# Kernel tuning notes

Hardware: AMD Instinct MI355X
Metric: run time of the kernel (lower is better)

The kernel has to match this reference:

```python
import jax, jax.numpy as jnp
import numpy as np

D_IN, D, K, N_CLASSES = 384, 512, 6, 2
SCALE = D ** (-0.5)

def _linear_params(key, fan_in, fan_out):
    kw, kb = jax.random.split(key)
    w = jax.random.normal(kw, (fan_in, fan_out), jnp.float32) * 0.02
    b = jax.random.normal(kb, (fan_out,), jnp.float32) * 0.01
    return w, b

def setup_inputs() -> dict:
    key = jax.random.key(0)
    ks = jax.random.split(key, 10)
    x = jax.random.normal(ks[0], (16384, D_IN), jnp.float32)
    fc1_w, fc1_b = _linear_params(ks[1], D_IN, D)
    wh_w, wh_b = _linear_params(ks[2], D, D)
    wt_w, wt_b = _linear_params(ks[3], D, D)
    lin1_w, lin1_b = _linear_params(ks[4], D, D)
    lin2_w, lin2_b = _linear_params(ks[5], D, D)
    att1_w, att1_b = _linear_params(ks[6], D, D // 2)
    att2_w, att2_b = _linear_params(ks[7], D // 2, 1)
    ln_g = jnp.ones((D,), jnp.float32)
    ln_b = jnp.zeros((D,), jnp.float32)
    fc_w, fc_b = _linear_params(ks[8], D, N_CLASSES)
    return dict(x=x, fc1_w=fc1_w, fc1_b=fc1_b, wh_w=wh_w, wh_b=wh_b,
                wt_w=wt_w, wt_b=wt_b, lin1_w=lin1_w, lin1_b=lin1_b,
                lin2_w=lin2_w, lin2_b=lin2_b, att1_w=att1_w, att1_b=att1_b,
                att2_w=att2_w, att2_b=att2_b, ln_g=ln_g, ln_b=ln_b,
                fc_w=fc_w, fc_b=fc_b)

def _forward(x, fc1_w, fc1_b, wh_w, wh_b, wt_w, wt_b, lin1_w, lin1_b,
             lin2_w, lin2_b, att1_w, att1_b, att2_w, att2_b, ln_g, ln_b,
             fc_w, fc_b):
    lrelu = jax.nn.leaky_relu  # slope 0.01, matches nn.LeakyReLU default
    h = lrelu(x @ fc1_w + fc1_b)                    # [N, D]
    h = (h + h.mean(axis=0, keepdims=True)) * 0.5
    e_h = h @ wh_w + wh_b                           # [N, D]
    e_t = h @ wt_w + wt_b                           # [N, D]
    attn_logit = (e_h * SCALE) @ e_t.T              # [N, N]
    topk_w, topk_i = jax.lax.top_k(attn_logit, K)   # [N, K]
    Nb = e_t[topk_i]                                # gather neighbors [N, K, D]
    p = jax.nn.softmax(topk_w, axis=-1)             # [N, K]
    eh_r = p[..., None] * Nb + (1.0 - p)[..., None] * e_h[:, None, :]
    gate = jnp.tanh(e_h[:, None, :] + eh_r)         # [N, K, D]
    # faithful to torch.einsum('ijkl,ijkm->ijk', Nb, gate): product of sums
    ka_w = Nb.sum(axis=-1) * gate.sum(axis=-1)      # [N, K]
    ka_p = jax.nn.softmax(ka_w, axis=-1)
    e_Nh = jnp.einsum('nk,nkd->nd', ka_p, Nb)       # [N, D]
    sum_emb = lrelu((e_h + e_Nh) @ lin1_w + lin1_b)
    bi_emb = lrelu((e_h * e_Nh) @ lin2_w + lin2_b)
    emb = sum_emb + bi_emb                          # [N, D] (dropout=eval, identity)
    # GlobalAttention readout
    a = lrelu(emb @ att1_w + att1_b) @ att2_w + att2_b  # [N, 1]
    g = jax.nn.softmax(a, axis=0)
    pooled = (g * emb).sum(axis=0, keepdims=True)   # [1, D]
    mu = pooled.mean(axis=-1, keepdims=True)
    var = pooled.var(axis=-1, keepdims=True)
    normed = (pooled - mu) * jax.lax.rsqrt(var + 1e-5) * ln_g + ln_b
    logits = normed @ fc_w + fc_b                   # [1, n_classes]
    return logits

def reference(x, fc1_w, fc1_b, wh_w, wh_b, wt_w, wt_b, lin1_w, lin1_b,
              lin2_w, lin2_b, att1_w, att1_b, att2_w, att2_b, ln_g, ln_b,
              fc_w, fc_b):
    logits = _forward(x, fc1_w, fc1_b, wh_w, wh_b, wt_w, wt_b, lin1_w, lin1_b,
                      lin2_w, lin2_b, att1_w, att1_b, att2_w, att2_b,
                      ln_g, ln_b, fc_w, fc_b)
    y_prob = jax.nn.softmax(logits, axis=-1)
    return logits, y_prob
```

## Files before the change

### kernel.cpp

```cpp
#include <hip/hip_runtime.h>
#include <math.h>

#define NROWS 16384
#define DIN   384
#define DIM   512
#define KSEL  6
#define NSPLIT 4
#define COLS_PER_SPLIT (NROWS / NSPLIT)
#define ATT_SCALE 0.044194173824159216f

typedef unsigned short u16;
typedef __attribute__((ext_vector_type(8))) short bf16x8;
typedef __attribute__((ext_vector_type(16))) float f32x16;

static __device__ __forceinline__ float lrelu_f(float v) {
  return v > 0.f ? v : 0.01f * v;
}

static __device__ __forceinline__ u16 f2bf(float f) {
  unsigned u = __float_as_uint(f);
  unsigned r = (u + 0x7FFFu + ((u >> 16) & 1u)) >> 16;
  return (u16)r;
}

static __device__ __forceinline__ float bf2f(u16 v) {
  return __uint_as_float(((unsigned)v) << 16);
}

static __device__ __forceinline__ void sbar() {
  asm volatile("" ::: "memory");
  __builtin_amdgcn_s_barrier();
  asm volatile("" ::: "memory");
}

static __device__ __forceinline__ void wconv_body(const float* W, u16* Wt,
                                                  int K, int N, int t) {
  if (t >= K * N) return;
  int k = t / N, n = t - k * N;
  Wt[(size_t)n * K + k] = f2bf(W[t]);
}

__global__ __launch_bounds__(256)
void prep(const float* __restrict__ X, u16* __restrict__ Xb,
          const float* __restrict__ fc1_w, u16* __restrict__ fc1t,
          const float* __restrict__ wh_w, u16* __restrict__ wht,
          const float* __restrict__ wt_w, u16* __restrict__ wtt,
          const float* __restrict__ lin1_w, u16* __restrict__ lin1t,
          const float* __restrict__ lin2_w, u16* __restrict__ lin2t,
          const float* __restrict__ att1_w, u16* __restrict__ att1t) {
  const int b = blockIdx.x, tid = threadIdx.x;
  if (b < 3072) {
    int i = b * 256 + tid;
    const float4* p = (const float4*)X + (size_t)i * 2;
    float4 a = p[0], c = p[1];
    uint4 o;
    o.x = f2bf(a.x) | ((unsigned)f2bf(a.y) << 16);
    o.y = f2bf(a.z) | ((unsigned)f2bf(a.w) << 16);
    o.z = f2bf(c.x) | ((unsigned)f2bf(c.y) << 16);
    o.w = f2bf(c.z) | ((unsigned)f2bf(c.w) << 16);
    ((uint4*)Xb)[i] = o;
  } else if (b < 3840) {
    wconv_body(fc1_w, fc1t, 384, 512, (b - 3072) * 256 + tid);
  } else if (b < 4864) {
    wconv_body(wh_w, wht, 512, 512, (b - 3840) * 256 + tid);
  } else if (b < 5888) {
    wconv_body(wt_w, wtt, 512, 512, (b - 4864) * 256 + tid);
  } else if (b < 6912) {
    wconv_body(lin1_w, lin1t, 512, 512, (b - 5888) * 256 + tid);
  } else if (b < 7936) {
    wconv_body(lin2_w, lin2t, 512, 512, (b - 6912) * 256 + tid);
  } else {
    wconv_body(att1_w, att1t, 512, 256, (b - 7936) * 256 + tid);
  }
}

__global__ __launch_bounds__(256)
void colsum_partial(const float* __restrict__ H, float* __restrict__ part) {
  int col = blockIdx.x * 64 + (threadIdx.x & 63);
  int sub = threadIdx.x >> 6;
  int rEnd = blockIdx.y * 512 + 512;
  float s = 0.f;
  for (int r = blockIdx.y * 512 + sub; r < rEnd; r += 4)
    s += H[(size_t)r * DIM + col];
  __shared__ float sh[4][64];
  sh[sub][threadIdx.x & 63] = s;
  __syncthreads();
  if (threadIdx.x < 64) {
    float tot = sh[0][threadIdx.x] + sh[1][threadIdx.x] +
                sh[2][threadIdx.x] + sh[3][threadIdx.x];
    part[(size_t)blockIdx.y * DIM + col] = tot;
  }
}

__global__ void finalize_mean(const float* __restrict__ part,
                              float* __restrict__ mean) {
  int c = threadIdx.x;
  float s = 0.f;
  for (int j = 0; j < 32; j++) s += part[j * DIM + c];
  mean[c] = s * (1.0f / NROWS);
}

__global__ __launch_bounds__(256)
void h_fix_bf(const float* __restrict__ H0, const float* __restrict__ mean,
              u16* __restrict__ Hb) {
  int idx = blockIdx.x * 256 + threadIdx.x;
  int c = (idx * 8) & (DIM - 1);
  const float4* p = (const float4*)H0 + (size_t)idx * 2;
  float4 a = p[0], b = p[1];
  float4 m0 = *(const float4*)(mean + c);
  float4 m1 = *(const float4*)(mean + c + 4);
  a.x = (a.x + m0.x) * 0.5f; a.y = (a.y + m0.y) * 0.5f;
  a.z = (a.z + m0.z) * 0.5f; a.w = (a.w + m0.w) * 0.5f;
  b.x = (b.x + m1.x) * 0.5f; b.y = (b.y + m1.y) * 0.5f;
  b.z = (b.z + m1.z) * 0.5f; b.w = (b.w + m1.w) * 0.5f;
  uint4 o;
  o.x = f2bf(a.x) | ((unsigned)f2bf(a.y) << 16);
  o.y = f2bf(a.z) | ((unsigned)f2bf(a.w) << 16);
  o.z = f2bf(b.x) | ((unsigned)f2bf(b.y) << 16);
  o.w = f2bf(b.z) | ((unsigned)f2bf(b.w) << 16);
  ((uint4*)Hb)[idx] = o;
}

template<int ACT, int STOREBF, int STOREF32>
__global__ __launch_bounds__(256, 2)
void gemm_bf16(const u16* __restrict__ A, const u16* __restrict__ Wt,
               const float* __restrict__ bias, float* __restrict__ C,
               u16* __restrict__ Cb, float bscale, int K, int N) {
  __shared__ char lds[65536];
  const int tid = threadIdx.x;
  const int w = tid >> 6, l = tid & 63;
  const int l31 = l & 31, lh = l >> 5, lh16 = lh << 4;
  const int qg = w & 1, ng = w >> 1;
  const int swz = (l31 & 7) << 4;
  const int rowBase = blockIdx.y * 128;
  const int colBase = blockIdx.x * 128;
  const int nsteps = K >> 6;

  f32x16 z;
  #pragma unroll
  for (int i = 0; i < 16; i++) z[i] = 0.f;
  f32x16 acc00 = z, acc01 = z, acc10 = z, acc11 = z;

#define GSTAGE(buf_, kc_) do { \
    const int r_ = tid >> 3, j_ = tid & 7; \
    const int js_ = ((j_ ^ (r_ & 7)) << 3); \
    const u16* as_ = A + (size_t)rowBase * K + (kc_); \
    const u16* ws_ = Wt + (size_t)colBase * K + (kc_); \
    char* ab_ = lds + (buf_) * 16384; \
    char* wb_ = lds + 32768 + (buf_) * 16384; \
    _Pragma("unroll") \
    for (int p_ = 0; p_ < 4; ++p_) { \
      __builtin_amdgcn_global_load_lds( \
        (const __attribute__((address_space(1))) void*)(as_ + (size_t)(r_ + 32 * p_) * K + js_), \
        (__attribute__((address_space(3))) void*)(ab_ + w * 1024 + p_ * 4096), 16, 0, 0); \
      __builtin_amdgcn_global_load_lds( \
        (const __attribute__((address_space(1))) void*)(ws_ + (size_t)(r_ + 32 * p_) * K + js_), \
        (__attribute__((address_space(3))) void*)(wb_ + w * 1024 + p_ * 4096), 16, 0, 0); \
    } \
  } while (0)

  GSTAGE(0, 0);
  asm volatile("s_waitcnt vmcnt(0)" ::: "memory");
  sbar();
  #pragma unroll 1
  for (int s = 0; s < nsteps; ++s) {
    const int cur = s & 1;
    if (s + 1 < nsteps) GSTAGE(cur ^ 1, (s + 1) * 64);
    __builtin_amdgcn_sched_barrier(0);
    const char* ab = lds + cur * 16384;
    const char* wb = lds + 32768 + cur * 16384;
    __builtin_amdgcn_s_setprio(1);
    #pragma unroll
    for (int s4 = 0; s4 < 4; ++s4) {
      const int off = (s4 * 32 + lh16) ^ swz;
      bf16x8 am0 = *(const bf16x8*)(ab + (qg * 64 + l31) * 128 + off);
      bf16x8 am1 = *(const bf16x8*)(ab + (qg * 64 + 32 + l31) * 128 + off);
      bf16x8 wn0 = *(const bf16x8*)(wb + (ng * 64 + l31) * 128 + off);
      bf16x8 wn1 = *(const bf16x8*)(wb + (ng * 64 + 32 + l31) * 128 + off);
      acc00 = __builtin_amdgcn_mfma_f32_32x32x16_bf16(wn0, am0, acc00, 0, 0, 0);
      acc01 = __builtin_amdgcn_mfma_f32_32x32x16_bf16(wn1, am0, acc01, 0, 0, 0);
      acc10 = __builtin_amdgcn_mfma_f32_32x32x16_bf16(wn0, am1, acc10, 0, 0, 0);
      acc11 = __builtin_amdgcn_mfma_f32_32x32x16_bf16(wn1, am1, acc11, 0, 0, 0);
    }
    __builtin_amdgcn_s_setprio(0);
    asm volatile("s_waitcnt vmcnt(0)" ::: "memory");
    sbar();
  }
#undef GSTAGE

  float* Ls = (float*)lds;
  {
    const int m0 = qg * 64 + l31;
    const int k0 = (m0 & 7) << 2;
    #pragma unroll
    for (int r = 0; r < 16; ++r) {
      const int nd = ng * 64 + (r & 3) + 8 * (r >> 2) + 4 * lh;
      Ls[m0 * 128 + (nd ^ k0)] = acc00[r];
      Ls[m0 * 128 + ((nd + 32) ^ k0)] = acc01[r];
      Ls[(m0 + 32) * 128 + (nd ^ k0)] = acc10[r];
      Ls[(m0 + 32) * 128 + ((nd + 32) ^ k0)] = acc11[r];
    }
  }
  sbar();
  #pragma unroll
  for (int p = 0; p < 16; ++p) {
    int idx = tid + 256 * p;
    int m = idx >> 5, c4 = (idx & 31) << 2;
    float4 v = *(const float4*)&Ls[m * 128 + (c4 ^ ((m & 7) << 2))];
    int col = colBase + c4;
    float4 bv = *(const float4*)&bias[col];
    v.x += bv.x; v.y += bv.y; v.z += bv.z; v.w += bv.w;
    if (ACT) {
      v.x = lrelu_f(v.x); v.y = lrelu_f(v.y);
      v.z = lrelu_f(v.z); v.w = lrelu_f(v.w);
    }
    size_t o = (size_t)(rowBase + m) * N + col;
    if (STOREF32) *(float4*)&C[o] = v;
    if (STOREBF) {
      ushort4 q;
      q.x = f2bf(v.x * bscale); q.y = f2bf(v.y * bscale);
      q.z = f2bf(v.z * bscale); q.w = f2bf(v.w * bscale);
      *(ushort4*)&Cb[o] = q;
    }
  }
}

__global__ __launch_bounds__(256, 2)
void gemm_dualA(const u16* __restrict__ A, const u16* __restrict__ W1t,
                const u16* __restrict__ W2t,
                const float* __restrict__ b1, const float* __restrict__ b2,
                u16* __restrict__ C1b, u16* __restrict__ C2b) {
  __shared__ char lds[65536];
  const int tid = threadIdx.x;
  const int w = tid >> 6, l = tid & 63;
  const int l31 = l & 31, lh = l >> 5, lh16 = lh << 4;
  const int qg = w & 1, ng = w >> 1;
  const int swz = (l31 & 7) << 4;
  const int rowBase = blockIdx.y * 128;
  const int colBase = blockIdx.x * 128;

  f32x16 z;
  #pragma unroll
  for (int i = 0; i < 16; i++) z[i] = 0.f;
  f32x16 p00 = z, p01 = z, p10 = z, p11 = z;
  f32x16 q00 = z, q01 = z, q10 = z, q11 = z;

  #pragma unroll 1
  for (int s = 0; s < 8; ++s) {
    {
      const int r_ = tid >> 3, j_ = tid & 7;
      const int js_ = ((j_ ^ (r_ & 7)) << 3);
      const u16* as_ = A + (size_t)rowBase * DIM + s * 64;
      const u16* w1_ = W1t + (size_t)colBase * DIM + s * 64;
      const u16* w2_ = W2t + (size_t)colBase * DIM + s * 64;
      #pragma unroll
      for (int p_ = 0; p_ < 4; ++p_) {
        __builtin_amdgcn_global_load_lds(
          (const __attribute__((address_space(1))) void*)(as_ + (size_t)(r_ + 32 * p_) * DIM + js_),
          (__attribute__((address_space(3))) void*)(lds + w * 1024 + p_ * 4096), 16, 0, 0);
        __builtin_amdgcn_global_load_lds(
          (const __attribute__((address_space(1))) void*)(w1_ + (size_t)(r_ + 32 * p_) * DIM + js_),
          (__attribute__((address_space(3))) void*)(lds + 16384 + w * 1024 + p_ * 4096), 16, 0, 0);
        __builtin_amdgcn_global_load_lds(
          (const __attribute__((address_space(1))) void*)(w2_ + (size_t)(r_ + 32 * p_) * DIM + js_),
          (__attribute__((address_space(3))) void*)(lds + 32768 + w * 1024 + p_ * 4096), 16, 0, 0);
      }
    }
    asm volatile("s_waitcnt vmcnt(0)" ::: "memory");
    sbar();
    const char* ab = lds;
    const char* w1b = lds + 16384;
    const char* w2b = lds + 32768;
    __builtin_amdgcn_s_setprio(1);
    #pragma unroll
    for (int s4 = 0; s4 < 4; ++s4) {
      const int off = (s4 * 32 + lh16) ^ swz;
      bf16x8 am0 = *(const bf16x8*)(ab + (qg * 64 + l31) * 128 + off);
      bf16x8 am1 = *(const bf16x8*)(ab + (qg * 64 + 32 + l31) * 128 + off);
      bf16x8 x0 = *(const bf16x8*)(w1b + (ng * 64 + l31) * 128 + off);
      bf16x8 x1 = *(const bf16x8*)(w1b + (ng * 64 + 32 + l31) * 128 + off);
      bf16x8 y0 = *(const bf16x8*)(w2b + (ng * 64 + l31) * 128 + off);
      bf16x8 y1 = *(const bf16x8*)(w2b + (ng * 64 + 32 + l31) * 128 + off);
      p00 = __builtin_amdgcn_mfma_f32_32x32x16_bf16(x0, am0, p00, 0, 0, 0);
      p01 = __builtin_amdgcn_mfma_f32_32x32x16_bf16(x1, am0, p01, 0, 0, 0);
      p10 = __builtin_amdgcn_mfma_f32_32x32x16_bf16(x0, am1, p10, 0, 0, 0);
      p11 = __builtin_amdgcn_mfma_f32_32x32x16_bf16(x1, am1, p11, 0, 0, 0);
      q00 = __builtin_amdgcn_mfma_f32_32x32x16_bf16(y0, am0, q00, 0, 0, 0);
      q01 = __builtin_amdgcn_mfma_f32_32x32x16_bf16(y1, am0, q01, 0, 0, 0);
      q10 = __builtin_amdgcn_mfma_f32_32x32x16_bf16(y0, am1, q10, 0, 0, 0);
      q11 = __builtin_amdgcn_mfma_f32_32x32x16_bf16(y1, am1, q11, 0, 0, 0);
    }
    __builtin_amdgcn_s_setprio(0);
    sbar();
  }

  float* Ls = (float*)lds;
  const int m0 = qg * 64 + l31;
  const int k0 = (m0 & 7) << 2;
  #pragma unroll
  for (int r = 0; r < 16; ++r) {
    const int nd = ng * 64 + (r & 3) + 8 * (r >> 2) + 4 * lh;
    Ls[m0 * 128 + (nd ^ k0)] = p00[r];
    Ls[m0 * 128 + ((nd + 32) ^ k0)] = p01[r];
    Ls[(m0 + 32) * 128 + (nd ^ k0)] = p10[r];
    Ls[(m0 + 32) * 128 + ((nd + 32) ^ k0)] = p11[r];
  }
  sbar();
  #pragma unroll
  for (int p = 0; p < 16; ++p) {
    int idx = tid + 256 * p;
    int m = idx >> 5, c4 = (idx & 31) << 2;
    float4 v = *(const float4*)&Ls[m * 128 + (c4 ^ ((m & 7) << 2))];
    int col = colBase + c4;
    float4 bv = *(const float4*)&b1[col];
    v.x += bv.x; v.y += bv.y; v.z += bv.z; v.w += bv.w;
    size_t o = (size_t)(rowBase + m) * DIM + col;
    ushort4 qo;
    qo.x = f2bf(v.x); qo.y = f2bf(v.y); qo.z = f2bf(v.z); qo.w = f2bf(v.w);
    *(ushort4*)&C1b[o] = qo;
  }
  sbar();
  #pragma unroll
  for (int r = 0; r < 16; ++r) {
    const int nd = ng * 64 + (r & 3) + 8 * (r >> 2) + 4 * lh;
    Ls[m0 * 128 + (nd ^ k0)] = q00[r];
    Ls[m0 * 128 + ((nd + 32) ^ k0)] = q01[r];
    Ls[(m0 + 32) * 128 + (nd ^ k0)] = q10[r];
    Ls[(m0 + 32) * 128 + ((nd + 32) ^ k0)] = q11[r];
  }
  sbar();
  #pragma unroll
  for (int p = 0; p < 16; ++p) {
    int idx = tid + 256 * p;
    int m = idx >> 5, c4 = (idx & 31) << 2;
    float4 v = *(const float4*)&Ls[m * 128 + (c4 ^ ((m & 7) << 2))];
    int col = colBase + c4;
    float4 bv = *(const float4*)&b2[col];
    v.x += bv.x; v.y += bv.y; v.z += bv.z; v.w += bv.w;
    size_t o = (size_t)(rowBase + m) * DIM + col;
    ushort4 qo;
    qo.x = f2bf(v.x); qo.y = f2bf(v.y); qo.z = f2bf(v.z); qo.w = f2bf(v.w);
    *(ushort4*)&C2b[o] = qo;
  }
}

__global__ __launch_bounds__(256, 2)
void gemm_dualsum(const u16* __restrict__ A1, const u16* __restrict__ A2,
                  const u16* __restrict__ W1t, const u16* __restrict__ W2t,
                  const float* __restrict__ b1, const float* __restrict__ b2,
                  u16* __restrict__ Cb) {
  __shared__ char lds[65536];
  const int tid = threadIdx.x;
  const int w = tid >> 6, l = tid & 63;
  const int l31 = l & 31, lh = l >> 5, lh16 = lh << 4;
  const int qg = w & 1, ng = w >> 1;
  const int swz = (l31 & 7) << 4;
  const int rowBase = blockIdx.y * 128;
  const int colBase = blockIdx.x * 128;

  f32x16 z;
  #pragma unroll
  for (int i = 0; i < 16; i++) z[i] = 0.f;
  f32x16 p00 = z, p01 = z, p10 = z, p11 = z;
  f32x16 q00 = z, q01 = z, q10 = z, q11 = z;

  #pragma unroll 1
  for (int s = 0; s < 8; ++s) {
    {
      const int r_ = tid >> 3, j_ = tid & 7;
      const int js_ = ((j_ ^ (r_ & 7)) << 3);
      const u16* a1_ = A1 + (size_t)rowBase * DIM + s * 64;
      const u16* a2_ = A2 + (size_t)rowBase * DIM + s * 64;
      const u16* w1_ = W1t + (size_t)colBase * DIM + s * 64;
      const u16* w2_ = W2t + (size_t)colBase * DIM + s * 64;
      #pragma unroll
      for (int p_ = 0; p_ < 4; ++p_) {
        __builtin_amdgcn_global_load_lds(
          (const __attribute__((address_space(1))) void*)(a1_ + (size_t)(r_ + 32 * p_) * DIM + js_),
          (__attribute__((address_space(3))) void*)(lds + w * 1024 + p_ * 4096), 16, 0, 0);
        __builtin_amdgcn_global_load_lds(
          (const __attribute__((address_space(1))) void*)(a2_ + (size_t)(r_ + 32 * p_) * DIM + js_),
          (__attribute__((address_space(3))) void*)(lds + 16384 + w * 1024 + p_ * 4096), 16, 0, 0);
        __builtin_amdgcn_global_load_lds(
          (const __attribute__((address_space(1))) void*)(w1_ + (size_t)(r_ + 32 * p_) * DIM + js_),
          (__attribute__((address_space(3))) void*)(lds + 32768 + w * 1024 + p_ * 4096), 16, 0, 0);
        __builtin_amdgcn_global_load_lds(
          (const __attribute__((address_space(1))) void*)(w2_ + (size_t)(r_ + 32 * p_) * DIM + js_),
          (__attribute__((address_space(3))) void*)(lds + 49152 + w * 1024 + p_ * 4096), 16, 0, 0);
      }
    }
    asm volatile("s_waitcnt vmcnt(0)" ::: "memory");
    sbar();
    const char* a1b = lds;
    const char* a2b = lds + 16384;
    const char* w1b = lds + 32768;
    const char* w2b = lds + 49152;
    __builtin_amdgcn_s_setprio(1);
    #pragma unroll
    for (int s4 = 0; s4 < 4; ++s4) {
      const int off = (s4 * 32 + lh16) ^ swz;
      bf16x8 am0 = *(const bf16x8*)(a1b + (qg * 64 + l31) * 128 + off);
      bf16x8 am1 = *(const bf16x8*)(a1b + (qg * 64 + 32 + l31) * 128 + off);
      bf16x8 bm0 = *(const bf16x8*)(a2b + (qg * 64 + l31) * 128 + off);
      bf16x8 bm1 = *(const bf16x8*)(a2b + (qg * 64 + 32 + l31) * 128 + off);
      bf16x8 x0 = *(const bf16x8*)(w1b + (ng * 64 + l31) * 128 + off);
      bf16x8 x1 = *(const bf16x8*)(w1b + (ng * 64 + 32 + l31) * 128 + off);
      bf16x8 y0 = *(const bf16x8*)(w2b + (ng * 64 + l31) * 128 + off);
      bf16x8 y1 = *(const bf16x8*)(w2b + (ng * 64 + 32 + l31) * 128 + off);
      p00 = __builtin_amdgcn_mfma_f32_32x32x16_bf16(x0, am0, p00, 0, 0, 0);
      p01 = __builtin_amdgcn_mfma_f32_32x32x16_bf16(x1, am0, p01, 0, 0, 0);
      p10 = __builtin_amdgcn_mfma_f32_32x32x16_bf16(x0, am1, p10, 0, 0, 0);
      p11 = __builtin_amdgcn_mfma_f32_32x32x16_bf16(x1, am1, p11, 0, 0, 0);
      q00 = __builtin_amdgcn_mfma_f32_32x32x16_bf16(y0, bm0, q00, 0, 0, 0);
      q01 = __builtin_amdgcn_mfma_f32_32x32x16_bf16(y1, bm0, q01, 0, 0, 0);
      q10 = __builtin_amdgcn_mfma_f32_32x32x16_bf16(y0, bm1, q10, 0, 0, 0);
      q11 = __builtin_amdgcn_mfma_f32_32x32x16_bf16(y1, bm1, q11, 0, 0, 0);
    }
    __builtin_amdgcn_s_setprio(0);
    sbar();
  }

  float* Ls = (float*)lds;
  const int m0 = qg * 64 + l31;
  const int k0 = (m0 & 7) << 2;
  #pragma unroll
  for (int r = 0; r < 16; ++r) {
    const int nd = ng * 64 + (r & 3) + 8 * (r >> 2) + 4 * lh;
    const int c0 = colBase + nd, c1 = colBase + nd + 32;
    Ls[m0 * 128 + (nd ^ k0)] =
        lrelu_f(p00[r] + b1[c0]) + lrelu_f(q00[r] + b2[c0]);
    Ls[m0 * 128 + ((nd + 32) ^ k0)] =
        lrelu_f(p01[r] + b1[c1]) + lrelu_f(q01[r] + b2[c1]);
    Ls[(m0 + 32) * 128 + (nd ^ k0)] =
        lrelu_f(p10[r] + b1[c0]) + lrelu_f(q10[r] + b2[c0]);
    Ls[(m0 + 32) * 128 + ((nd + 32) ^ k0)] =
        lrelu_f(p11[r] + b1[c1]) + lrelu_f(q11[r] + b2[c1]);
  }
  sbar();
  #pragma unroll
  for (int p = 0; p < 16; ++p) {
    int idx = tid + 256 * p;
    int m = idx >> 5, c4 = (idx & 31) << 2;
    float4 v = *(const float4*)&Ls[m * 128 + (c4 ^ ((m & 7) << 2))];
    int col = colBase + c4;
    size_t o = (size_t)(rowBase + m) * DIM + col;
    ushort4 qo;
    qo.x = f2bf(v.x); qo.y = f2bf(v.y); qo.z = f2bf(v.z); qo.w = f2bf(v.w);
    *(ushort4*)&Cb[o] = qo;
  }
}

#define T6(tv, tix, vv, cc) do { float v_ = (vv); \
  if (v_ > tv[5]) { tv[5] = v_; tix[5] = (cc); \
    if (tv[5] > tv[4]) { float t=tv[4];tv[4]=tv[5];tv[5]=t; int q=tix[4];tix[4]=tix[5];tix[5]=q; } \
    if (tv[4] > tv[3]) { float t=tv[3];tv[3]=tv[4];tv[4]=t; int q=tix[3];tix[3]=tix[4];tix[4]=q; } \
    if (tv[3] > tv[2]) { float t=tv[2];tv[2]=tv[3];tv[3]=t; int q=tix[2];tix[2]=tix[3];tix[3]=q; } \
    if (tv[2] > tv[1]) { float t=tv[1];tv[1]=tv[2];tv[2]=t; int q=tix[1];tix[1]=tix[2];tix[2]=q; } \
    if (tv[1] > tv[0]) { float t=tv[0];tv[0]=tv[1];tv[1]=t; int q=tix[0];tix[0]=tix[1];tix[1]=q; } \
  } } while (0)

__global__ __launch_bounds__(256, 2)
void attn_topk_mfma(const u16* __restrict__ EHb, const u16* __restrict__ ETb,
                    float* __restrict__ TWp, int* __restrict__ TIp) {
  __shared__ char lds[49152];
  const int tid = threadIdx.x;
  const int w = tid >> 6, l = tid & 63;
  const int l31 = l & 31, lh = l >> 5;

  const int bid = blockIdx.x;
  const int xcd = bid & 7;
  const int split = xcd & 3;
  const int rowBase = ((xcd >> 2) * 64 + (bid >> 3)) * 128;
  const int qrow = rowBase + w * 32 + l31;

  bf16x8 areg[32];
  {
    const u16* ap = EHb + (size_t)qrow * DIM + lh * 8;
    #pragma unroll
    for (int ks = 0; ks < 32; ++ks)
      areg[ks] = *(const bf16x8*)(ap + ks * 16);
  }

  f32x16 z;
  #pragma unroll
  for (int i = 0; i < 16; i++) z[i] = 0.f;
  f32x16 acc0 = z, acc1 = z;

  float tv[KSEL]; int tix[KSEL];
  #pragma unroll
  for (int k = 0; k < KSEL; k++) { tv[k] = -INFINITY; tix[k] = 0x7fffffff; }

#define STAGE(bufi_, ph_) do { \
    const int ct_ = (ph_) >> 2, kc_ = (ph_) & 3; \
    char* db_ = lds + (bufi_) * 16384; \
    const u16* bs_ = ETb + (size_t)(split * COLS_PER_SPLIT + ct_ * 64) * DIM + kc_ * 128; \
    _Pragma("unroll") \
    for (int p_ = 0; p_ < 4; ++p_) { \
      const int c_ = (w * 4 + p_) * 64 + l; \
      const int rn_ = c_ >> 4; \
      const int js_ = ((c_ & 15) ^ (rn_ & 15)) << 3; \
      __builtin_amdgcn_global_load_lds( \
        (const __attribute__((address_space(1))) void*)(bs_ + (size_t)rn_ * DIM + js_), \
        (__attribute__((address_space(3))) void*)(db_ + (w * 4 + p_) * 1024), 16, 0, 0); \
    } \
  } while (0)

  int bufr = 0;
  STAGE(0, 0);
  STAGE(1, 1);
  asm volatile("s_waitcnt vmcnt(4)" ::: "memory");

  #pragma unroll 1
  for (int ct = 0; ct < 64; ++ct) {
    #pragma unroll
    for (int kc = 0; kc < 4; ++kc) {
      sbar();
      const char* db = lds + bufr * 16384;
      __builtin_amdgcn_s_setprio(1);
      #pragma unroll
      for (int s = 0; s < 8; ++s) {
        const int j0 = ((s * 2 + lh) ^ (l31 & 15)) * 16;
        bf16x8 bn0 = *(const bf16x8*)(db + l31 * 256 + j0);
        const int r1 = 32 + l31;
        const int j1 = ((s * 2 + lh) ^ (r1 & 15)) * 16;
        bf16x8 bn1 = *(const bf16x8*)(db + r1 * 256 + j1);
        acc0 = __builtin_amdgcn_mfma_f32_32x32x16_bf16(bn0, areg[kc * 8 + s], acc0, 0, 0, 0);
        acc1 = __builtin_amdgcn_mfma_f32_32x32x16_bf16(bn1, areg[kc * 8 + s], acc1, 0, 0, 0);
      }
      __builtin_amdgcn_s_setprio(0);
      if (kc == 3) {
        const int cb = split * COLS_PER_SPLIT + ct * 64 + 4 * lh;
        #pragma unroll
        for (int r = 0; r < 16; ++r) {
          const int nd = cb + (r & 3) + 8 * (r >> 2);
          T6(tv, tix, acc0[r], nd);
          T6(tv, tix, acc1[r], nd + 32);
        }
        acc0 = z; acc1 = z;
      }
      __builtin_amdgcn_sched_barrier(0);
      {
        const int p = ct * 4 + kc;
        if (p + 2 < 256) {
          const int bs = (bufr >= 1) ? bufr - 1 : bufr + 2;
          STAGE(bs, p + 2);
        }
        if (p < 254) { asm volatile("s_waitcnt vmcnt(4)" ::: "memory"); }
        else         { asm volatile("s_waitcnt vmcnt(0)" ::: "memory"); }
      }
      bufr = (bufr == 2) ? 0 : bufr + 1;
    }
  }
#undef STAGE

  {
    float pv[KSEL]; int pi[KSEL];
    #pragma unroll
    for (int k = 0; k < KSEL; k++) {
      pv[k] = __shfl_xor(tv[k], 32);
      pi[k] = __shfl_xor(tix[k], 32);
    }
    #pragma unroll
    for (int k = 0; k < KSEL; k++) {
      float cv = pv[k]; int ci = pi[k];
      if ((cv > tv[5]) || (cv == tv[5] && ci < tix[5])) {
        tv[5] = cv; tix[5] = ci;
        if ((tv[5] > tv[4]) || (tv[5] == tv[4] && tix[5] < tix[4])) {
          float t = tv[4]; tv[4] = tv[5]; tv[5] = t;
          int q = tix[4]; tix[4] = tix[5]; tix[5] = q; }
        if ((tv[4] > tv[3]) || (tv[4] == tv[3] && tix[4] < tix[3])) {
          float t = tv[3]; tv[3] = tv[4]; tv[4] = t;
          int q = tix[3]; tix[3] = tix[4]; tix[4] = q; }
        if ((tv[3] > tv[2]) || (tv[3] == tv[2] && tix[3] < tix[2])) {
          float t = tv[2]; tv[2] = tv[3]; tv[3] = t;
          int q = tix[2]; tix[2] = tix[3]; tix[3] = q; }
        if ((tv[2] > tv[1]) || (tv[2] == tv[1] && tix[2] < tix[1])) {
          float t = tv[1]; tv[1] = tv[2]; tv[2] = t;
          int q = tix[1]; tix[1] = tix[2]; tix[2] = q; }
        if ((tv[1] > tv[0]) || (tv[1] == tv[0] && tix[1] < tix[0])) {
          float t = tv[0]; tv[0] = tv[1]; tv[1] = t;
          int q = tix[0]; tix[0] = tix[1]; tix[1] = q; }
      }
    }
  }
  if (lh == 0) {
    size_t o = ((size_t)split * NROWS + qrow) * KSEL;
    #pragma unroll
    for (int k = 0; k < KSEL; k++) {
      TWp[o + k] = tv[k] * ATT_SCALE;
      TIp[o + k] = tix[k];
    }
  }
}

__global__ __launch_bounds__(256)
void neighbor_kernel(const u16* __restrict__ EHb, const u16* __restrict__ ETb,
                     const float* __restrict__ TWp, const int* __restrict__ TIp,
                     u16* __restrict__ SINb, u16* __restrict__ BINb) {
  const int lane = threadIdx.x & 63;
  const int row = blockIdx.x * 4 + (threadIdx.x >> 6);
  const u16* eh = EHb + (size_t)row * DIM;
  float ehv[8];
  #pragma unroll
  for (int u = 0; u < 8; u++) ehv[u] = bf2f(eh[u * 64 + lane]);

  float tw[KSEL]; int ti[KSEL];
  #pragma unroll
  for (int k = 0; k < KSEL; k++) { tw[k] = -INFINITY; ti[k] = 0x7fffffff; }
  #pragma unroll
  for (int s = 0; s < NSPLIT; s++) {
    size_t o = ((size_t)s * NROWS + row) * KSEL;
    #pragma unroll
    for (int k = 0; k < KSEL; k++) {
      float cv = TWp[o + k]; int ci = TIp[o + k];
      if ((cv > tw[5]) || (cv == tw[5] && ci < ti[5])) {
        tw[5] = cv; ti[5] = ci;
        if ((tw[5] > tw[4]) || (tw[5] == tw[4] && ti[5] < ti[4])) {
          float t = tw[4]; tw[4] = tw[5]; tw[5] = t;
          int q = ti[4]; ti[4] = ti[5]; ti[5] = q; }
        if ((tw[4] > tw[3]) || (tw[4] == tw[3] && ti[4] < ti[3])) {
          float t = tw[3]; tw[3] = tw[4]; tw[4] = t;
          int q = ti[3]; ti[3] = ti[4]; ti[4] = q; }
        if ((tw[3] > tw[2]) || (tw[3] == tw[2] && ti[3] < ti[2])) {
          float t = tw[2]; tw[2] = tw[3]; tw[3] = t;
          int q = ti[2]; ti[2] = ti[3]; ti[3] = q; }
        if ((tw[2] > tw[1]) || (tw[2] == tw[1] && ti[2] < ti[1])) {
          float t = tw[1]; tw[1] = tw[2]; tw[2] = t;
          int q = ti[1]; ti[1] = ti[2]; ti[2] = q; }
        if ((tw[1] > tw[0]) || (tw[1] == tw[0] && ti[1] < ti[0])) {
          float t = tw[0]; tw[0] = tw[1]; tw[1] = t;
          int q = ti[0]; ti[0] = ti[1]; ti[1] = q; }
      }
    }
  }

  float m = tw[0];
  #pragma unroll
  for (int k = 1; k < KSEL; k++) m = fmaxf(m, tw[k]);
  float p[KSEL], ps = 0.f;
  #pragma unroll
  for (int k = 0; k < KSEL; k++) { p[k] = expf(tw[k] - m); ps += p[k]; }
  float inv = 1.f / ps;
  #pragma unroll
  for (int k = 0; k < KSEL; k++) p[k] *= inv;

  float nb[KSEL][8];
  float kaw[KSEL];
  #pragma unroll
  for (int k = 0; k < KSEL; k++) {
    const u16* et = ETb + (size_t)ti[k] * DIM;
    float snb = 0.f, sg = 0.f;
    #pragma unroll
    for (int u = 0; u < 8; u++) {
      float nbv = bf2f(et[u * 64 + lane]);
      nb[k][u] = nbv;
      float ehr = p[k] * nbv + (1.f - p[k]) * ehv[u];
      float g = tanhf(ehv[u] + ehr);
      snb += nbv; sg += g;
    }
    #pragma unroll
    for (int off = 32; off > 0; off >>= 1) {
      snb += __shfl_xor(snb, off);
      sg  += __shfl_xor(sg, off);
    }
    kaw[k] = snb * sg;
  }
  float km = kaw[0];
  #pragma unroll
  for (int k = 1; k < KSEL; k++) km = fmaxf(km, kaw[k]);
  float kp[KSEL], ks = 0.f;
  #pragma unroll
  for (int k = 0; k < KSEL; k++) { kp[k] = expf(kaw[k] - km); ks += kp[k]; }
  float kinv = 1.f / ks;
  #pragma unroll
  for (int k = 0; k < KSEL; k++) kp[k] *= kinv;

  #pragma unroll
  for (int u = 0; u < 8; u++) {
    float enh = 0.f;
    #pragma unroll
    for (int k = 0; k < KSEL; k++) enh += kp[k] * nb[k][u];
    size_t o = (size_t)row * DIM + u * 64 + lane;
    SINb[o] = f2bf(ehv[u] + enh);
    BINb[o] = f2bf(ehv[u] * enh);
  }
}

__global__ __launch_bounds__(256)
void att2_kernel(const u16* __restrict__ HIDb, const float* __restrict__ w2,
                 const float* __restrict__ b2, float* __restrict__ ASC) {
  const int lane = threadIdx.x & 63;
  const int row = blockIdx.x * 4 + (threadIdx.x >> 6);
  ushort4 hv = ((const ushort4*)(HIDb + (size_t)row * 256))[lane];
  float4 wv = ((const float4*)w2)[lane];
  float s = bf2f(hv.x) * wv.x + bf2f(hv.y) * wv.y +
            bf2f(hv.z) * wv.z + bf2f(hv.w) * wv.w;
  #pragma unroll
  for (int off = 32; off > 0; off >>= 1) s += __shfl_xor(s, off);
  if (lane == 0) ASC[row] = s + b2[0];
}

__global__ __launch_bounds__(1024)
void areduce(const float* __restrict__ ASC, float* __restrict__ stats) {
  __shared__ float sm[1024];
  int t = threadIdx.x;
  float m = -INFINITY;
  for (int i = t; i < NROWS; i += 1024) m = fmaxf(m, ASC[i]);
  sm[t] = m; __syncthreads();
  for (int s = 512; s > 0; s >>= 1) {
    if (t < s) sm[t] = fmaxf(sm[t], sm[t + s]);
    __syncthreads();
  }
  float mx = sm[0]; __syncthreads();
  float sum = 0.f;
  for (int i = t; i < NROWS; i += 1024) sum += expf(ASC[i] - mx);
  sm[t] = sum; __syncthreads();
  for (int s = 512; s > 0; s >>= 1) {
    if (t < s) sm[t] += sm[t + s];
    __syncthreads();
  }
  if (t == 0) { stats[0] = mx; stats[1] = sm[0]; }
}

__global__ __launch_bounds__(256)
void pooled_partial(const u16* __restrict__ EMBb, const float* __restrict__ ASC,
                    const float* __restrict__ stats, float* __restrict__ part) {
  int col = blockIdx.x * 64 + (threadIdx.x & 63);
  int sub = threadIdx.x >> 6;
  float mx = stats[0];
  int rEnd = blockIdx.y * 512 + 512;
  float s = 0.f;
  for (int r = blockIdx.y * 512 + sub; r < rEnd; r += 4)
    s += expf(ASC[r] - mx) * bf2f(EMBb[(size_t)r * DIM + col]);
  __shared__ float sh[4][64];
  sh[sub][threadIdx.x & 63] = s;
  __syncthreads();
  if (threadIdx.x < 64) {
    float tot = sh[0][threadIdx.x] + sh[1][threadIdx.x] +
                sh[2][threadIdx.x] + sh[3][threadIdx.x];
    part[(size_t)blockIdx.y * DIM + col] = tot;
  }
}

__global__ __launch_bounds__(512)
void final_kernel(const float* __restrict__ part, const float* __restrict__ stats,
                  const float* __restrict__ ln_g, const float* __restrict__ ln_b,
                  const float* __restrict__ fc_w, const float* __restrict__ fc_b,
                  float* __restrict__ out) {
  __shared__ float sh[512];
  int t = threadIdx.x;
  float s = 0.f;
  for (int j = 0; j < 32; j++) s += part[j * DIM + t];
  float pooled = s / stats[1];
  sh[t] = pooled; __syncthreads();
  for (int off = 256; off > 0; off >>= 1) {
    if (t < off) sh[t] += sh[t + off];
    __syncthreads();
  }
  float mu = sh[0] * (1.f / DIM); __syncthreads();
  float dv = pooled - mu;
  sh[t] = dv * dv; __syncthreads();
  for (int off = 256; off > 0; off >>= 1) {
    if (t < off) sh[t] += sh[t + off];
    __syncthreads();
  }
  float var = sh[0] * (1.f / DIM); __syncthreads();
  float normed = dv * rsqrtf(var + 1e-5f) * ln_g[t] + ln_b[t];
  sh[t] = normed * fc_w[t * 2 + 0]; __syncthreads();
  for (int off = 256; off > 0; off >>= 1) {
    if (t < off) sh[t] += sh[t + off];
    __syncthreads();
  }
  float l0 = sh[0] + fc_b[0]; __syncthreads();
  sh[t] = normed * fc_w[t * 2 + 1]; __syncthreads();
  for (int off = 256; off > 0; off >>= 1) {
    if (t < off) sh[t] += sh[t + off];
    __syncthreads();
  }
  float l1 = sh[0] + fc_b[1];
  if (t == 0) {
    float mm = fmaxf(l0, l1);
    float e0 = expf(l0 - mm), e1 = expf(l1 - mm);
    float si = 1.f / (e0 + e1);
    out[0] = l0; out[1] = l1; out[2] = e0 * si; out[3] = e1 * si;
  }
}

extern "C" void kernel_launch(void* const* d_in, const int* in_sizes, int n_in,
                              void* d_out, int out_size, void* d_ws, size_t ws_size,
                              hipStream_t stream) {
  (void)in_sizes; (void)n_in; (void)out_size; (void)ws_size;
  const float* x      = (const float*)d_in[0];
  const float* fc1_w  = (const float*)d_in[1];
  const float* fc1_b  = (const float*)d_in[2];
  const float* wh_w   = (const float*)d_in[3];
  const float* wh_b   = (const float*)d_in[4];
  const float* wt_w   = (const float*)d_in[5];
  const float* wt_b   = (const float*)d_in[6];
  const float* lin1_w = (const float*)d_in[7];
  const float* lin1_b = (const float*)d_in[8];
  const float* lin2_w = (const float*)d_in[9];
  const float* lin2_b = (const float*)d_in[10];
  const float* att1_w = (const float*)d_in[11];
  const float* att1_b = (const float*)d_in[12];
  const float* att2_w = (const float*)d_in[13];
  const float* att2_b = (const float*)d_in[14];
  const float* ln_g   = (const float*)d_in[15];
  const float* ln_b   = (const float*)d_in[16];
  const float* fc_w   = (const float*)d_in[17];
  const float* fc_b   = (const float*)d_in[18];
  float* out = (float*)d_out;

  char* ws = (char*)d_ws;
  float* B0   = (float*)(ws);
  u16*   sinb = (u16*)(ws + 33554432);
  u16*   binb = (u16*)(ws + 67108864);
  float* TWp  = (float*)(ws + 100663296);
  int*   TIp  = (int*)  (ws + 100663296 + 1572864);
  float* part = (float*)(ws + 100663296 + 3145728 + 786432);
  float* mean = (float*)(ws + 100663296 + 3145728 + 786432 + 65536);
  float* ascr = (float*)(ws + 100663296 + 3145728 + 786432 + 65536 + 2048);
  float* stats= (float*)(ws + 100663296 + 3145728 + 786432 + 65536 + 2048 + 65536);
  u16*   hb   = (u16*)(ws + 104732672);
  u16*   EHb  = (u16*)(ws + 104732672 + 16777216);
  u16*   ETb  = (u16*)(ws + 104732672 + 33554432);
  u16*   WT   = (u16*)(ws + 104732672 + 50331648);
  u16* fc1t = WT;
  u16* wht  = fc1t + 196608;
  u16* wtt  = wht + 262144;
  u16* lin1t= wtt + 262144;
  u16* lin2t= lin1t + 262144;
  u16* att1t= lin2t + 262144;
  u16* xb   = sinb;
  u16* embb = hb;
  u16* HIDb = EHb;

  prep<<<8448, 256, 0, stream>>>(x, xb, fc1_w, fc1t, wh_w, wht, wt_w, wtt,
                                 lin1_w, lin1t, lin2_w, lin2t, att1_w, att1t);
  gemm_bf16<1,0,1><<<dim3(4,128), 256, 0, stream>>>(xb, fc1t, fc1_b, B0, nullptr, 1.f, 384, 512);
  colsum_partial<<<dim3(8,32), 256, 0, stream>>>(B0, part);
  finalize_mean<<<1, 512, 0, stream>>>(part, mean);
  h_fix_bf<<<4096, 256, 0, stream>>>(B0, mean, hb);
  gemm_dualA<<<dim3(4,128), 256, 0, stream>>>(hb, wht, wtt, wh_b, wt_b, EHb, ETb);
  attn_topk_mfma<<<512, 256, 0, stream>>>(EHb, ETb, TWp, TIp);
  neighbor_kernel<<<4096, 256, 0, stream>>>(EHb, ETb, TWp, TIp, sinb, binb);
  gemm_dualsum<<<dim3(4,128), 256, 0, stream>>>(sinb, binb, lin1t, lin2t,
                                                lin1_b, lin2_b, embb);
  gemm_bf16<1,1,0><<<dim3(2,128), 256, 0, stream>>>(embb, att1t, att1_b, nullptr, HIDb, 1.f, 512, 256);
  att2_kernel<<<4096, 256, 0, stream>>>(HIDb, att2_w, att2_b, ascr);
  areduce<<<1, 1024, 0, stream>>>(ascr, stats);
  pooled_partial<<<dim3(8,32), 256, 0, stream>>>(embb, ascr, stats, part);
  final_kernel<<<1, 512, 0, stream>>>(part, stats, ln_g, ln_b, fc_w, fc_b, out);
}
```

Measured before the change: 592.9 us.

## Fuse att2 dot product into att1 GEMM and store fc1 output as bf16

After: 593.1 us. No clear change (+0.0%).

```diff
diff --git a/kernel.cpp b/kernel.cpp
--- a/kernel.cpp
+++ b/kernel.cpp
@@ -75,13 +75,13 @@
 }
 
 __global__ __launch_bounds__(256)
-void colsum_partial(const float* __restrict__ H, float* __restrict__ part) {
+void colsum_partial(const u16* __restrict__ H, float* __restrict__ part) {
   int col = blockIdx.x * 64 + (threadIdx.x & 63);
   int sub = threadIdx.x >> 6;
   int rEnd = blockIdx.y * 512 + 512;
   float s = 0.f;
   for (int r = blockIdx.y * 512 + sub; r < rEnd; r += 4)
-    s += H[(size_t)r * DIM + col];
+    s += bf2f(H[(size_t)r * DIM + col]);
   __shared__ float sh[4][64];
   sh[sub][threadIdx.x & 63] = s;
   __syncthreads();
@@ -101,31 +101,34 @@
 }
 
 __global__ __launch_bounds__(256)
-void h_fix_bf(const float* __restrict__ H0, const float* __restrict__ mean,
+void h_fix_bf(const u16* __restrict__ H0b, const float* __restrict__ mean,
               u16* __restrict__ Hb) {
   int idx = blockIdx.x * 256 + threadIdx.x;
   int c = (idx * 8) & (DIM - 1);
-  const float4* p = (const float4*)H0 + (size_t)idx * 2;
-  float4 a = p[0], b = p[1];
+  uint4 hv = ((const uint4*)H0b)[idx];
   float4 m0 = *(const float4*)(mean + c);
   float4 m1 = *(const float4*)(mean + c + 4);
-  a.x = (a.x + m0.x) * 0.5f; a.y = (a.y + m0.y) * 0.5f;
-  a.z = (a.z + m0.z) * 0.5f; a.w = (a.w + m0.w) * 0.5f;
-  b.x = (b.x + m1.x) * 0.5f; b.y = (b.y + m1.y) * 0.5f;
-  b.z = (b.z + m1.z) * 0.5f; b.w = (b.w + m1.w) * 0.5f;
+  float v0 = (bf2f((u16)(hv.x & 0xffff)) + m0.x) * 0.5f;
+  float v1 = (bf2f((u16)(hv.x >> 16))    + m0.y) * 0.5f;
+  float v2 = (bf2f((u16)(hv.y & 0xffff)) + m0.z) * 0.5f;
+  float v3 = (bf2f((u16)(hv.y >> 16))    + m0.w) * 0.5f;
+  float v4 = (bf2f((u16)(hv.z & 0xffff)) + m1.x) * 0.5f;
+  float v5 = (bf2f((u16)(hv.z >> 16))    + m1.y) * 0.5f;
+  float v6 = (bf2f((u16)(hv.w & 0xffff)) + m1.z) * 0.5f;
+  float v7 = (bf2f((u16)(hv.w >> 16))    + m1.w) * 0.5f;
   uint4 o;
-  o.x = f2bf(a.x) | ((unsigned)f2bf(a.y) << 16);
-  o.y = f2bf(a.z) | ((unsigned)f2bf(a.w) << 16);
-  o.z = f2bf(b.x) | ((unsigned)f2bf(b.y) << 16);
-  o.w = f2bf(b.z) | ((unsigned)f2bf(b.w) << 16);
+  o.x = f2bf(v0) | ((unsigned)f2bf(v1) << 16);
+  o.y = f2bf(v2) | ((unsigned)f2bf(v3) << 16);
+  o.z = f2bf(v4) | ((unsigned)f2bf(v5) << 16);
+  o.w = f2bf(v6) | ((unsigned)f2bf(v7) << 16);
   ((uint4*)Hb)[idx] = o;
 }
 
-template<int ACT, int STOREBF, int STOREF32>
+template<int ACT>
 __global__ __launch_bounds__(256, 2)
 void gemm_bf16(const u16* __restrict__ A, const u16* __restrict__ Wt,
-               const float* __restrict__ bias, float* __restrict__ C,
-               u16* __restrict__ Cb, float bscale, int K, int N) {
+               const float* __restrict__ bias, u16* __restrict__ Cb,
+               int K, int N) {
   __shared__ char lds[65536];
   const int tid = threadIdx.x;
   const int w = tid >> 6, l = tid & 63;
@@ -215,13 +218,122 @@
       v.z = lrelu_f(v.z); v.w = lrelu_f(v.w);
     }
     size_t o = (size_t)(rowBase + m) * N + col;
-    if (STOREF32) *(float4*)&C[o] = v;
-    if (STOREBF) {
-      ushort4 q;
-      q.x = f2bf(v.x * bscale); q.y = f2bf(v.y * bscale);
-      q.z = f2bf(v.z * bscale); q.w = f2bf(v.w * bscale);
-      *(ushort4*)&Cb[o] = q;
-    }
+    ushort4 q;
+    q.x = f2bf(v.x); q.y = f2bf(v.y); q.z = f2bf(v.z); q.w = f2bf(v.w);
+    *(ushort4*)&Cb[o] = q;
+  }
+}
+
+__global__ __launch_bounds__(256, 2)
+void gemm_att(const u16* __restrict__ A, const u16* __restrict__ Wt,
+              const float* __restrict__ b1, const float* __restrict__ w2,
+              const float* __restrict__ b2, float* __restrict__ ASC) {
+  __shared__ char lds[65536];
+  const int tid = threadIdx.x;
+  const int w = tid >> 6, l = tid & 63;
+  const int l31 = l & 31, lh = l >> 5, lh16 = lh << 4;
+  const int qg = w & 1, ng = w >> 1;
+  const int swz = (l31 & 7) << 4;
+  const int rowBase = blockIdx.x * 128;
+
+  float dot[16];
+  #pragma unroll
+  for (int i = 0; i < 16; i++) dot[i] = 0.f;
+
+  #pragma unroll 1
+  for (int ct = 0; ct < 2; ++ct) {
+    const int colBase = ct * 128;
+    f32x16 z;
+    #pragma unroll
+    for (int i = 0; i < 16; i++) z[i] = 0.f;
+    f32x16 acc00 = z, acc01 = z, acc10 = z, acc11 = z;
+
+#define GSTAGE2(buf_, kc_) do { \
+    const int r_ = tid >> 3, j_ = tid & 7; \
+    const int js_ = ((j_ ^ (r_ & 7)) << 3); \
+    const u16* as_ = A + (size_t)rowBase * DIM + (kc_); \
+    const u16* ws_ = Wt + (size_t)colBase * DIM + (kc_); \
+    char* ab_ = lds + (buf_) * 16384; \
+    char* wb_ = lds + 32768 + (buf_) * 16384; \
+    _Pragma("unroll") \
+    for (int p_ = 0; p_ < 4; ++p_) { \
+      __builtin_amdgcn_global_load_lds( \
+        (const __attribute__((address_space(1))) void*)(as_ + (size_t)(r_ + 32 * p_) * DIM + js_), \
+        (__attribute__((address_space(3))) void*)(ab_ + w * 1024 + p_ * 4096), 16, 0, 0); \
+      __builtin_amdgcn_global_load_lds( \
+        (const __attribute__((address_space(1))) void*)(ws_ + (size_t)(r_ + 32 * p_) * DIM + js_), \
+        (__attribute__((address_space(3))) void*)(wb_ + w * 1024 + p_ * 4096), 16, 0, 0); \
+    } \
+  } while (0)
+
+    GSTAGE2(0, 0);
+    asm volatile("s_waitcnt vmcnt(0)" ::: "memory");
+    sbar();
+    #pragma unroll 1
+    for (int s = 0; s < 8; ++s) {
+      const int cur = s & 1;
+      if (s + 1 < 8) GSTAGE2(cur ^ 1, (s + 1) * 64);
+      __builtin_amdgcn_sched_barrier(0);
+      const char* ab = lds + cur * 16384;
+      const char* wb = lds + 32768 + cur * 16384;
+      __builtin_amdgcn_s_setprio(1);
+      #pragma unroll
+      for (int s4 = 0; s4 < 4; ++s4) {
+        const int off = (s4 * 32 + lh16) ^ swz;
+        bf16x8 am0 = *(const bf16x8*)(ab + (qg * 64 + l31) * 128 + off);
+        bf16x8 am1 = *(const bf16x8*)(ab + (qg * 64 + 32 + l31) * 128 + off);
+        bf16x8 wn0 = *(const bf16x8*)(wb + (ng * 64 + l31) * 128 + off);
+        bf16x8 wn1 = *(const bf16x8*)(wb + (ng * 64 + 32 + l31) * 128 + off);
+        acc00 = __builtin_amdgcn_mfma_f32_32x32x16_bf16(wn0, am0, acc00, 0, 0, 0);
+        acc01 = __builtin_amdgcn_mfma_f32_32x32x16_bf16(wn1, am0, acc01, 0, 0, 0);
+        acc10 = __builtin_amdgcn_mfma_f32_32x32x16_bf16(wn0, am1, acc10, 0, 0, 0);
+        acc11 = __builtin_amdgcn_mfma_f32_32x32x16_bf16(wn1, am1, acc11, 0, 0, 0);
+      }
+      __builtin_amdgcn_s_setprio(0);
+      asm volatile("s_waitcnt vmcnt(0)" ::: "memory");
+      sbar();
+    }
+#undef GSTAGE2
+
+    float* Ls = (float*)lds;
+    {
+      const int m0 = qg * 64 + l31;
+      const int k0 = (m0 & 7) << 2;
+      #pragma unroll
+      for (int r = 0; r < 16; ++r) {
+        const int nd = ng * 64 + (r & 3) + 8 * (r >> 2) + 4 * lh;
+        Ls[m0 * 128 + (nd ^ k0)] = acc00[r];
+        Ls[m0 * 128 + ((nd + 32) ^ k0)] = acc01[r];
+        Ls[(m0 + 32) * 128 + (nd ^ k0)] = acc10[r];
+        Ls[(m0 + 32) * 128 + ((nd + 32) ^ k0)] = acc11[r];
+      }
+    }
+    sbar();
+    #pragma unroll
+    for (int p = 0; p < 16; ++p) {
+      int idx = tid + 256 * p;
+      int m = idx >> 5, c4 = (idx & 31) << 2;
+      float4 v = *(const float4*)&Ls[m * 128 + (c4 ^ ((m & 7) << 2))];
+      int col = colBase + c4;
+      float4 bv = *(const float4*)&b1[col];
+      float4 wv = *(const float4*)&w2[col];
+      v.x = lrelu_f(v.x + bv.x); v.y = lrelu_f(v.y + bv.y);
+      v.z = lrelu_f(v.z + bv.z); v.w = lrelu_f(v.w + bv.w);
+      dot[p] += v.x * wv.x + v.y * wv.y + v.z * wv.z + v.w * wv.w;
+    }
+    sbar();
+  }
+
+  #pragma unroll
+  for (int p = 0; p < 16; ++p) {
+    float v = dot[p];
+    v += __shfl_xor(v, 16);
+    v += __shfl_xor(v, 8);
+    v += __shfl_xor(v, 4);
+    v += __shfl_xor(v, 2);
+    v += __shfl_xor(v, 1);
+    if (l31 == 0)
+      ASC[rowBase + 8 * p + (tid >> 5)] = v + b2[0];
   }
 }
 
@@ -686,20 +798,6 @@
   }
 }
 
-__global__ __launch_bounds__(256)
-void att2_kernel(const u16* __restrict__ HIDb, const float* __restrict__ w2,
-                 const float* __restrict__ b2, float* __restrict__ ASC) {
-  const int lane = threadIdx.x & 63;
-  const int row = blockIdx.x * 4 + (threadIdx.x >> 6);
-  ushort4 hv = ((const ushort4*)(HIDb + (size_t)row * 256))[lane];
-  float4 wv = ((const float4*)w2)[lane];
-  float s = bf2f(hv.x) * wv.x + bf2f(hv.y) * wv.y +
-            bf2f(hv.z) * wv.z + bf2f(hv.w) * wv.w;
-  #pragma unroll
-  for (int off = 32; off > 0; off >>= 1) s += __shfl_xor(s, off);
-  if (lane == 0) ASC[row] = s + b2[0];
-}
-
 __global__ __launch_bounds__(1024)
 void areduce(const float* __restrict__ ASC, float* __restrict__ stats) {
   __shared__ float sm[1024];
@@ -812,7 +910,7 @@
   float* out = (float*)d_out;
 
   char* ws = (char*)d_ws;
-  float* B0   = (float*)(ws);
+  u16*   h0b  = (u16*)(ws);
   u16*   sinb = (u16*)(ws + 33554432);
   u16*   binb = (u16*)(ws + 67108864);
   float* TWp  = (float*)(ws + 100663296);
@@ -833,21 +931,19 @@
   u16* att1t= lin2t + 262144;
   u16* xb   = sinb;
   u16* embb = hb;
-  u16* HIDb = EHb;
 
   prep<<<8448, 256, 0, stream>>>(x, xb, fc1_w, fc1t, wh_w, wht, wt_w, wtt,
                                  lin1_w, lin1t, lin2_w, lin2t, att1_w, att1t);
-  gemm_bf16<1,0,1><<<dim3(4,128), 256, 0, stream>>>(xb, fc1t, fc1_b, B0, nullptr, 1.f, 384, 512);
-  colsum_partial<<<dim3(8,32), 256, 0, stream>>>(B0, part);
+  gemm_bf16<1><<<dim3(4,128), 256, 0, stream>>>(xb, fc1t, fc1_b, h0b, 384, 512);
+  colsum_partial<<<dim3(8,32), 256, 0, stream>>>(h0b, part);
   finalize_mean<<<1, 512, 0, stream>>>(part, mean);
-  h_fix_bf<<<4096, 256, 0, stream>>>(B0, mean, hb);
+  h_fix_bf<<<4096, 256, 0, stream>>>(h0b, mean, hb);
   gemm_dualA<<<dim3(4,128), 256, 0, stream>>>(hb, wht, wtt, wh_b, wt_b, EHb, ETb);
   attn_topk_mfma<<<512, 256, 0, stream>>>(EHb, ETb, TWp, TIp);
   neighbor_kernel<<<4096, 256, 0, stream>>>(EHb, ETb, TWp, TIp, sinb, binb);
   gemm_dualsum<<<dim3(4,128), 256, 0, stream>>>(sinb, binb, lin1t, lin2t,
                                                 lin1_b, lin2_b, embb);
-  gemm_bf16<1,1,0><<<dim3(2,128), 256, 0, stream>>>(embb, att1t, att1_b, nullptr, HIDb, 1.f, 512, 256);
-  att2_kernel<<<4096, 256, 0, stream>>>(HIDb, att2_w, att2_b, ascr);
+  gemm_att<<<128, 256, 0, stream>>>(embb, att1t, att1_b, att2_w, att2_b, ascr);
   areduce<<<1, 1024, 0, stream>>>(ascr, stats);
   pooled_partial<<<dim3(8,32), 256, 0, stream>>>(embb, ascr, stats, part);
   final_kernel<<<1, 512, 0, stream>>>(part, stats, ln_g, ln_b, fc_w, fc_b, out);
```
